# Performance work log

Measured on AMD Instinct MI355X. Metric: run time of the kernel, lower is better.

Reference implementation:

```python
import jax, jax.numpy as jnp
import numpy as np

DIM = 512
HEADS = 8
LF, P = 32, 32
N = LF * P
LOC_DIM = 64  # loc_emd_dim == locf_dim == 64
SCALE = (DIM // HEADS) ** -0.5


def _position_matrix(boxes):
    # boxes: [N,4] x1y1x2y2 -> [N,N,4] relative geometry (relation-network style)
    x1, y1, x2, y2 = jnp.split(boxes, 4, axis=1)  # each [N,1]
    w = x2 - x1 + 1.0
    h = y2 - y1 + 1.0
    cx = 0.5 * (x1 + x2)
    cy = 0.5 * (y1 + y2)
    dx = jnp.log(jnp.maximum(jnp.abs((cx - cx.T) / w), 1e-3))
    dy = jnp.log(jnp.maximum(jnp.abs((cy - cy.T) / h), 1e-3))
    dw = jnp.log(w.T / w)
    dh = jnp.log(h.T / h)
    return jnp.stack([dx, dy, dw, dh], axis=-1)  # [N,N,4]


def _position_embedding(pos_mat, feat_dim=LOC_DIM, wave_length=1000.0):
    # pos_mat: [N,N,4] -> [N,N,feat_dim] sin/cos embedding
    nf = feat_dim // 8
    dim_mat = wave_length ** (jnp.arange(nf, dtype=jnp.float32) * (8.0 / feat_dim))  # [nf]
    div = pos_mat[..., None] * 100.0 / dim_mat  # [N,N,4,nf]
    emb = jnp.concatenate([jnp.sin(div), jnp.cos(div)], axis=-1)  # [N,N,4,2nf]
    return emb.reshape(pos_mat.shape[0], pos_mat.shape[1], feat_dim)


def setup_inputs() -> dict:
    key = jax.random.key(0)
    ks = jax.random.split(key, 8)
    x = jax.random.normal(ks[0], (1, N, DIM), jnp.float32)
    x_reg = jax.random.normal(ks[1], (1, N, DIM), jnp.float32)
    # valid boxes: x1y1x2y2 within a ~1000x600 frame
    cx = jax.random.uniform(ks[2], (LF, P, 1)) * 1000.0
    cy = jax.random.uniform(ks[3], (LF, P, 1)) * 600.0
    w = jax.random.uniform(ks[4], (LF, P, 1)) * 150.0 + 10.0
    h = jax.random.uniform(ks[5], (LF, P, 1)) * 150.0 + 10.0
    locs = jnp.concatenate([cx - w / 2, cy - h / 2, cx + w / 2, cy + h / 2], axis=-1)
    W_qkv = jax.random.normal(ks[6], (3 * DIM, DIM), jnp.float32) * 0.02
    W_loc = jax.random.normal(ks[7], (HEADS, LOC_DIM), jnp.float32) * 0.01  # 1x1 conv weight
    b_loc = jnp.zeros((HEADS,), jnp.float32)
    return {"x": x, "x_reg": x_reg, "locs": locs, "W_qkv": W_qkv, "W_loc": W_loc, "b_loc": b_loc}


def reference(x, x_reg, locs, W_qkv, W_loc, b_loc):
    B, n, C = x.shape
    boxes = locs.reshape(-1, 4)
    # location embedding -> 1x1 conv -> ReLU  (attn_lt: [H,N,N])
    pos_emb = _position_embedding(_position_matrix(boxes), LOC_DIM)  # [N,N,64]
    attn_lt = jax.nn.relu(jnp.einsum('nmf,hf->hnm', pos_emb, W_loc) + b_loc[:, None, None])
    # qkv projection (bias=False)
    qkv = (x @ W_qkv.T).reshape(B, n, 3, HEADS, C // HEADS)
    qkv = jnp.transpose(qkv, (2, 0, 3, 1, 4))  # [3,B,H,N,hd]
    q, k, v = qkv[0], qkv[1], qkv[2]
    attn = jnp.einsum('bhnd,bhmd->bhnm', q, k) * SCALE
    attn = attn + jnp.log(attn_lt + 1e-6)[None]  # loc_fuse_type == 'add'
    attn = jax.nn.softmax(attn, axis=-1)
    out = jnp.einsum('bhnm,bhmd->bhnd', attn, v)
    return jnp.transpose(out, (0, 2, 1, 3)).reshape(B, n, C)
```

## Files before the change

kernel.cpp:

```cpp
#include <hip/hip_runtime.h>
#include <hip/hip_bf16.h>


namespace {
constexpr int NN   = 1024;
constexpr int CDIM = 512;
constexpr int NH   = 8;
constexpr int HD   = 64;
constexpr int NOUT = 3 * CDIM;
constexpr int PROJ_BLOCKS = (NN / 64) * (NOUT / 64);
constexpr float QSCALE = 0.125f;

constexpr size_t QKBF_OFF_U16 = 0;
constexpr size_t VT_OFF_U16   = (size_t)2 * NH * NN * HD;
constexpr size_t XB_OFF_U16   = VT_OFF_U16 + (size_t)NH * HD * NN;
constexpr size_t WB_OFF_U16   = XB_OFF_U16 + (size_t)NN * CDIM;
constexpr size_t L_OFF_U16    = WB_OFF_U16 + (size_t)NOUT * CDIM;
constexpr size_t END_U16      = L_OFF_U16 + (size_t)NH * NN * NN;
constexpr size_t BF_OFF_F32   = END_U16 / 2;
constexpr size_t WR_OFF_F32   = BF_OFF_F32 + 6 * NN;
constexpr size_t W2_OFF_U16   = 2 * (WR_OFF_F32 + 528);
}

typedef __attribute__((ext_vector_type(8))) short short8v;
typedef __attribute__((ext_vector_type(4))) float f32x4;

__device__ __forceinline__ unsigned short f2bf(float f) {
  union { float f; unsigned int u; } v; v.f = f;
  unsigned int u = v.u;
  u += 0x7fffu + ((u >> 16) & 1u);
  return (unsigned short)(u >> 16);
}
__device__ __forceinline__ float b2f(unsigned short u) {
  union { unsigned int u; float f; } v; v.u = ((unsigned int)u) << 16; return v.f;
}

__global__ __launch_bounds__(256) void k_cvt(const float* __restrict__ x,
                                             const float* __restrict__ wq,
                                             const float* __restrict__ locs,
                                             const float* __restrict__ wloc,
                                             const float* __restrict__ bloc,
                                             unsigned short* __restrict__ xb,
                                             unsigned short* __restrict__ wb,
                                             float* __restrict__ bf,
                                             float* __restrict__ wr,
                                             unsigned short* __restrict__ w2) {
  constexpr int XTOT = NN * CDIM;
  constexpr int CVT_BLOCKS = 1280;
  int b = blockIdx.x;
  int tid = threadIdx.x;
  if (b < CVT_BLOCKS) {
    int idx = (b * 256 + tid) * 4;
    if (idx < XTOT) {
      float4 v = *reinterpret_cast<const float4*>(x + idx);
      ushort4 o;
      o.x = f2bf(v.x); o.y = f2bf(v.y); o.z = f2bf(v.z); o.w = f2bf(v.w);
      *reinterpret_cast<ushort4*>(xb + idx) = o;
    } else {
      int j = idx - XTOT;
      float4 v = *reinterpret_cast<const float4*>(wq + j);
      ushort4 o;
      o.x = f2bf(v.x); o.y = f2bf(v.y); o.z = f2bf(v.z); o.w = f2bf(v.w);
      *reinterpret_cast<ushort4*>(wb + j) = o;
    }
  } else {
    for (int i = tid; i < NN; i += 256) {
      float4 b4 = reinterpret_cast<const float4*>(locs)[i];
      float x1 = b4.x, y1 = b4.y, x2 = b4.z, y2 = b4.w;
      float w = x2 - x1 + 1.0f;
      float h = y2 - y1 + 1.0f;
      bf[0 * NN + i] = 0.5f * (x1 + x2);
      bf[1 * NN + i] = 0.5f * (y1 + y2);
      bf[2 * NN + i] = w;
      bf[3 * NN + i] = h;
      bf[4 * NN + i] = logf(w);
      bf[5 * NN + i] = logf(h);
    }
    if (tid < 8) wr[512 + tid] = bloc[tid];
    for (int i = tid; i < 16 * 64; i += 256) {
      int hh = i >> 6, f = i & 63;
      int sc = f & 1, tj = f >> 1, j = tj & 3, t = tj >> 2;
      float v = (hh < 8) ? wloc[hh * 64 + j * 16 + sc * 8 + t] : 0.0f;
      w2[i] = f2bf(v);
    }
  }
}

__global__ __launch_bounds__(256) void k_mid(const unsigned short* __restrict__ xb,
                                             const unsigned short* __restrict__ wb,
                                             unsigned short* __restrict__ qk_bf,
                                             unsigned short* __restrict__ vt,
                                             const float* __restrict__ bf,
                                             const float* __restrict__ wr,
                                             const unsigned short* __restrict__ w2,
                                             unsigned short* __restrict__ L) {
  __shared__ unsigned short A_lds[64][72];
  __shared__ unsigned short B_lds[64][72];
  int blk = blockIdx.x;
  int tid = threadIdx.x;

  if (blk >= PROJ_BLOCKS) {
    int blk2 = blk - PROJ_BLOCKS;
    int n = blk2 >> 2;
    int m0 = (blk2 & 3) * 256;
    int w = tid >> 6, l = tid & 63, g = l >> 4, c = l & 15;

    const float* cx = bf;
    const float* cy = bf + NN;
    const float* lw = bf + 4 * NN;
    const float* lh = bf + 5 * NN;

    float cxn = cx[n], cyn = cy[n];
    float rwn = 1.0f / bf[2 * NN + n];
    float rhn = 1.0f / bf[3 * NN + n];
    float lwn = lw[n], lhn = lh[n];

    float ang0 = 100.0f * exp2f(-1.2457230355894468f * (float)g);
    float ang1 = ang0 * 0.031622776601683794f;

    short8v aw_lo = *reinterpret_cast<const short8v*>(w2 + c * 64 + 8 * g);
    short8v aw_hi = *reinterpret_cast<const short8v*>(w2 + c * 64 + 32 + 8 * g);
    float br_[4];
#pragma unroll
    for (int r = 0; r < 4; ++r) br_[r] = wr[512 + ((4 * g + r) & 7)];

#pragma unroll
    for (int it = 0; it < 4; ++it) {
      int m = m0 + w * 64 + it * 16 + c;
      float dx = __logf(fmaxf(fabsf((cxn - cx[m]) * rwn), 1e-3f));
      float dy = __logf(fmaxf(fabsf((cyn - cy[m]) * rhn), 1e-3f));
      float dwv = lw[m] - lwn;
      float dhv = lh[m] - lhn;
      float pos[4] = {dx, dy, dwv, dhv};

      union BU { unsigned int u[4]; short8v v; } b0, b1;
#pragma unroll
      for (int j = 0; j < 4; ++j) {
        float s0v, c0v, s1v, c1v;
        __sincosf(pos[j] * ang0, &s0v, &c0v);
        __sincosf(pos[j] * ang1, &s1v, &c1v);
        union { __hip_bfloat162 h; unsigned int u; } cv0, cv1;
        cv0.h = __float22bfloat162_rn(make_float2(s0v, c0v));
        cv1.h = __float22bfloat162_rn(make_float2(s1v, c1v));
        b0.u[j] = cv0.u;
        b1.u[j] = cv1.u;
      }

      f32x4 z = {0.f, 0.f, 0.f, 0.f};
      f32x4 acc4 = __builtin_amdgcn_mfma_f32_16x16x32_bf16(aw_lo, b0.v, z, 0, 0, 0);
      acc4 = __builtin_amdgcn_mfma_f32_16x16x32_bf16(aw_hi, b1.v, acc4, 0, 0, 0);

      if (g < 2) {
#pragma unroll
        for (int r = 0; r < 4; ++r) {
          float v = fmaxf(acc4[r] + br_[r], 0.0f) + 1e-6f;
          L[((size_t)(4 * g + r) * NN + n) * NN + m] = f2bf(v);
        }
      }
    }
  } else {
    int t = blk;
    int n0 = (t & 15) * 64, i0 = (t >> 4) * 64;
    int w = tid >> 6, l = tid & 63, g = l >> 4, c = l & 15;
    int sr = tid >> 2;
    int sc = (tid & 3) * 16;

    f32x4 acc[4];
#pragma unroll
    for (int ct = 0; ct < 4; ++ct) acc[ct] = (f32x4){0.f, 0.f, 0.f, 0.f};

    for (int kt = 0; kt < CDIM; kt += 64) {
      const unsigned short* asrc = xb + (size_t)(n0 + sr) * CDIM + kt + sc;
      const unsigned short* bsrc = wb + (size_t)(i0 + sr) * CDIM + kt + sc;
      *reinterpret_cast<short8v*>(&A_lds[sr][sc])     = *reinterpret_cast<const short8v*>(asrc);
      *reinterpret_cast<short8v*>(&A_lds[sr][sc + 8]) = *reinterpret_cast<const short8v*>(asrc + 8);
      *reinterpret_cast<short8v*>(&B_lds[sr][sc])     = *reinterpret_cast<const short8v*>(bsrc);
      *reinterpret_cast<short8v*>(&B_lds[sr][sc + 8]) = *reinterpret_cast<const short8v*>(bsrc + 8);
      __syncthreads();
#pragma unroll
      for (int kks = 0; kks < 2; ++kks) {
        short8v a = *reinterpret_cast<const short8v*>(&A_lds[16 * w + c][kks * 32 + 8 * g]);
#pragma unroll
        for (int ct = 0; ct < 4; ++ct) {
          short8v b = *reinterpret_cast<const short8v*>(&B_lds[16 * ct + c][kks * 32 + 8 * g]);
          acc[ct] = __builtin_amdgcn_mfma_f32_16x16x32_bf16(a, b, acc[ct], 0, 0, 0);
        }
      }
      __syncthreads();
    }

    int s = i0 >> 9;
    int hh = (i0 >> 6) & 7;
    if (s < 2) {
      float scale = (s == 0) ? QSCALE : 1.0f;
      unsigned short* dst = qk_bf + ((size_t)(s * NH + hh) * NN) * HD;
#pragma unroll
      for (int ct = 0; ct < 4; ++ct)
#pragma unroll
        for (int r = 0; r < 4; ++r) {
          int n = n0 + 16 * w + 4 * g + r;
          dst[(size_t)n * HD + 16 * ct + c] = f2bf(acc[ct][r] * scale);
        }
    } else {
#pragma unroll
      for (int ct = 0; ct < 4; ++ct)
#pragma unroll
        for (int r = 0; r < 4; ++r) {
          A_lds[16 * w + 4 * g + r][16 * ct + c] = f2bf(acc[ct][r]);
        }
      __syncthreads();
      int d = tid >> 2;
      int nn0 = (tid & 3) * 16;
      unsigned short o[16];
#pragma unroll
      for (int nn = 0; nn < 16; ++nn) o[nn] = A_lds[nn0 + nn][d];
      unsigned short* dst = vt + ((size_t)hh * HD + d) * NN + n0 + nn0;
      *reinterpret_cast<short8v*>(dst)     = *reinterpret_cast<short8v*>(&o[0]);
      *reinterpret_cast<short8v*>(dst + 8) = *reinterpret_cast<short8v*>(&o[8]);
    }
  }
}

__global__ __launch_bounds__(512) void k_mha(const unsigned short* __restrict__ qk,
                                             const unsigned short* __restrict__ vt,
                                             const unsigned short* __restrict__ L,
                                             float* __restrict__ out) {
  __shared__ short8v smem16[3200];
  auto V = reinterpret_cast<unsigned short(*)[64][40]>(smem16);
  auto P = reinterpret_cast<unsigned short(*)[640]>(
      reinterpret_cast<char*>(smem16) + 40960);
  auto accs = reinterpret_cast<float(*)[16][68]>(smem16);
  auto mls = reinterpret_cast<float(*)[2][16]>(reinterpret_cast<char*>(smem16) + 34816);
  auto scw2 = reinterpret_cast<float(*)[16]>(reinterpret_cast<char*>(smem16) + 35840);
  auto rlf = reinterpret_cast<float*>(reinterpret_cast<char*>(smem16) + 36352);

  int tid = threadIdx.x;
  int w = tid >> 6;
  int l = tid & 63;
  int g = l >> 4;
  int c = l & 15;
  int h = blockIdx.y;
  int n0 = blockIdx.x * 16;

  const unsigned short* qb = qk + ((size_t)(0 * NH + h) * NN + n0) * HD;
  const unsigned short* kb = qk + ((size_t)(1 * NH + h) * NN) * HD;
  const unsigned short* vb = vt + (size_t)h * HD * NN;
  const unsigned short* Lb = L + ((size_t)h * NN + n0 + 4 * g) * NN;

  short8v a_lo = *reinterpret_cast<const short8v*>(qb + (size_t)c * HD + 8 * g);
  short8v a_hi = *reinterpret_cast<const short8v*>(qb + (size_t)c * HD + 32 + 8 * g);

  f32x4 acc[4];
#pragma unroll
  for (int ct = 0; ct < 4; ++ct) acc[ct] = (f32x4){0.f, 0.f, 0.f, 0.f};
  float m_run[4] = {-3.0e38f, -3.0e38f, -3.0e38f, -3.0e38f};
  float l_run[4] = {0.f, 0.f, 0.f, 0.f};

#pragma unroll
  for (int it = 0; it < 4; ++it) {
    int mt = w * 128 + it * 32;

#pragma unroll
    for (int p = 0; p < 4; ++p) {
      int d = p * 16 + (l >> 2);
      int key16 = (l & 3) * 8;
      *reinterpret_cast<short8v*>(&V[w][d][key16]) =
          *reinterpret_cast<const short8v*>(vb + (size_t)d * NN + mt + key16);
    }

    float t0[4], t1[4];
#pragma unroll
    for (int r = 0; r < 4; ++r) {
      t0[r] = b2f(Lb[(size_t)r * NN + mt + c]);
      t1[r] = b2f(Lb[(size_t)r * NN + mt + 16 + c]);
    }

    const unsigned short* k0p = kb + (size_t)(mt + c) * HD + 8 * g;
    const unsigned short* k1p = kb + (size_t)(mt + 16 + c) * HD + 8 * g;
    short8v b0_lo = *reinterpret_cast<const short8v*>(k0p);
    short8v b0_hi = *reinterpret_cast<const short8v*>(k0p + 32);
    short8v b1_lo = *reinterpret_cast<const short8v*>(k1p);
    short8v b1_hi = *reinterpret_cast<const short8v*>(k1p + 32);

    __builtin_amdgcn_s_setprio(1);
    f32x4 z = {0.f, 0.f, 0.f, 0.f};
    f32x4 s0 = __builtin_amdgcn_mfma_f32_16x16x32_bf16(a_lo, b0_lo, z, 0, 0, 0);
    s0 = __builtin_amdgcn_mfma_f32_16x16x32_bf16(a_hi, b0_hi, s0, 0, 0, 0);
    f32x4 s1 = __builtin_amdgcn_mfma_f32_16x16x32_bf16(a_lo, b1_lo, z, 0, 0, 0);
    s1 = __builtin_amdgcn_mfma_f32_16x16x32_bf16(a_hi, b1_hi, s1, 0, 0, 0);
    __builtin_amdgcn_s_setprio(0);

    float sc[4], p0[4], p1[4];
#pragma unroll
    for (int r = 0; r < 4; ++r) {
      float mx = fmaxf(s0[r], s1[r]);
      mx = fmaxf(mx, __shfl_xor(mx, 1));
      mx = fmaxf(mx, __shfl_xor(mx, 2));
      mx = fmaxf(mx, __shfl_xor(mx, 4));
      mx = fmaxf(mx, __shfl_xor(mx, 8));
      float m_new = fmaxf(m_run[r], mx);
      sc[r] = __expf(m_run[r] - m_new);
      p0[r] = t0[r] * __expf(s0[r] - m_new);
      p1[r] = t1[r] * __expf(s1[r] - m_new);
      l_run[r] = l_run[r] * sc[r] + (p0[r] + p1[r]);
      m_run[r] = m_new;
    }
#pragma unroll
    for (int ct = 0; ct < 4; ++ct)
#pragma unroll
      for (int r = 0; r < 4; ++r) acc[ct][r] *= sc[r];

#pragma unroll
    for (int r = 0; r < 4; ++r) {
      P[w][(4 * g + r) * 40 + c] = f2bf(p0[r]);
      P[w][(4 * g + r) * 40 + 16 + c] = f2bf(p1[r]);
    }
    __builtin_amdgcn_wave_barrier();

    short8v pa = *reinterpret_cast<const short8v*>(&P[w][c * 40 + 8 * g]);
    __builtin_amdgcn_s_setprio(1);
#pragma unroll
    for (int ct = 0; ct < 4; ++ct) {
      short8v vbf = *reinterpret_cast<const short8v*>(&V[w][ct * 16 + c][8 * g]);
      acc[ct] = __builtin_amdgcn_mfma_f32_16x16x32_bf16(pa, vbf, acc[ct], 0, 0, 0);
    }
    __builtin_amdgcn_s_setprio(0);
    __builtin_amdgcn_wave_barrier();
  }

#pragma unroll
  for (int r = 0; r < 4; ++r) {
    float ls = l_run[r];
    ls += __shfl_xor(ls, 1);
    ls += __shfl_xor(ls, 2);
    ls += __shfl_xor(ls, 4);
    ls += __shfl_xor(ls, 8);
    l_run[r] = ls;
  }

  __syncthreads();

  if (c == 0) {
#pragma unroll
    for (int r = 0; r < 4; ++r) {
      mls[w][0][4 * g + r] = m_run[r];
      mls[w][1][4 * g + r] = l_run[r];
    }
  }
#pragma unroll
  for (int ct = 0; ct < 4; ++ct)
#pragma unroll
    for (int r = 0; r < 4; ++r) accs[w][4 * g + r][ct * 16 + c] = acc[ct][r];
  __syncthreads();

  if (tid < 16) {
    int row = tid;
    float mfin = mls[0][0][row];
#pragma unroll
    for (int w2i = 1; w2i < 8; ++w2i) mfin = fmaxf(mfin, mls[w2i][0][row]);
    float lfin = 0.f;
#pragma unroll
    for (int w2i = 0; w2i < 8; ++w2i) {
      float scv = __expf(mls[w2i][0][row] - mfin);
      scw2[w2i][row] = scv;
      lfin += mls[w2i][1][row] * scv;
    }
    rlf[row] = 1.0f / lfin;
  }
  __syncthreads();

#pragma unroll
  for (int o = tid; o < 16 * 64; o += 512) {
    int row = o >> 6, col = o & 63;
    float val = 0.f;
#pragma unroll
    for (int w2i = 0; w2i < 8; ++w2i) {
      val += scw2[w2i][row] * accs[w2i][row][col];
    }
    out[(size_t)(n0 + row) * CDIM + h * HD + col] = val * rlf[row];
  }
}

extern "C" void kernel_launch(void* const* d_in, const int* in_sizes, int n_in,
                              void* d_out, int out_size, void* d_ws, size_t ws_size,
                              hipStream_t stream) {
  const float* x    = (const float*)d_in[0];
  const float* locs = (const float*)d_in[2];
  const float* wqkv = (const float*)d_in[3];
  const float* wloc = (const float*)d_in[4];
  const float* bloc = (const float*)d_in[5];
  float* out = (float*)d_out;
  float* ws = (float*)d_ws;
  unsigned short* ws_u16 = (unsigned short*)d_ws;

  unsigned short* qk_bf = ws_u16 + QKBF_OFF_U16;
  unsigned short* vt_bf = ws_u16 + VT_OFF_U16;
  unsigned short* xb    = ws_u16 + XB_OFF_U16;
  unsigned short* wb    = ws_u16 + WB_OFF_U16;
  unsigned short* L     = ws_u16 + L_OFF_U16;
  unsigned short* w2    = ws_u16 + W2_OFF_U16;
  float* bf = ws + BF_OFF_F32;
  float* wr = ws + WR_OFF_F32;

  k_cvt<<<dim3(1281), dim3(256), 0, stream>>>(x, wqkv, locs, wloc, bloc, xb, wb, bf, wr, w2);
  k_mid<<<dim3(PROJ_BLOCKS + 4096), dim3(256), 0, stream>>>(
      xb, wb, qk_bf, vt_bf, bf, wr, w2, L);
  k_mha<<<dim3(NN / 16, NH), dim3(512), 0, stream>>>(qk_bf, vt_bf, L, out);
}
```

Baseline: 50.36 us.

## Merge conversion and mid kernels into one launch with atomic flag dependency

Fuses the fp32-to-bf16 conversion kernel and the projection/location-embedding kernel into a single launch. Projection blocks spin on a global atomic counter until all conversion blocks finish, while location-embedding blocks run independently. Those blocks now compute box geometry and the conv weight layout inline from the raw inputs instead of from a precomputed buffer. The aim is to remove a launch boundary and let the location work overlap the conversion. In exchange it adds a memset, a spin-wait that depends on block scheduling order (the converters have lower block indices), and redundant per-block recomputation of logs and weights.

```diff
diff --git a/kernel.cpp b/kernel.cpp
--- a/kernel.cpp
+++ b/kernel.cpp
@@ -8,6 +8,8 @@
 constexpr int NH   = 8;
 constexpr int HD   = 64;
 constexpr int NOUT = 3 * CDIM;
+constexpr int CVT_BLOCKS  = 1280;
+constexpr int LOC_BLOCKS  = 4096;
 constexpr int PROJ_BLOCKS = (NN / 64) * (NOUT / 64);
 constexpr float QSCALE = 0.125f;
 
@@ -17,9 +19,7 @@
 constexpr size_t WB_OFF_U16   = XB_OFF_U16 + (size_t)NN * CDIM;
 constexpr size_t L_OFF_U16    = WB_OFF_U16 + (size_t)NOUT * CDIM;
 constexpr size_t END_U16      = L_OFF_U16 + (size_t)NH * NN * NN;
-constexpr size_t BF_OFF_F32   = END_U16 / 2;
-constexpr size_t WR_OFF_F32   = BF_OFF_F32 + 6 * NN;
-constexpr size_t W2_OFF_U16   = 2 * (WR_OFF_F32 + 528);
+constexpr size_t FLAG_OFF_B   = END_U16 * 2;
 }
 
 typedef __attribute__((ext_vector_type(8))) short short8v;
@@ -35,22 +35,25 @@
   union { unsigned int u; float f; } v; v.u = ((unsigned int)u) << 16; return v.f;
 }
 
-__global__ __launch_bounds__(256) void k_cvt(const float* __restrict__ x,
-                                             const float* __restrict__ wq,
-                                             const float* __restrict__ locs,
-                                             const float* __restrict__ wloc,
-                                             const float* __restrict__ bloc,
-                                             unsigned short* __restrict__ xb,
-                                             unsigned short* __restrict__ wb,
-                                             float* __restrict__ bf,
-                                             float* __restrict__ wr,
-                                             unsigned short* __restrict__ w2) {
-  constexpr int XTOT = NN * CDIM;
-  constexpr int CVT_BLOCKS = 1280;
-  int b = blockIdx.x;
+__global__ __launch_bounds__(256) void k_union(const float* __restrict__ x,
+                                               const float* __restrict__ wq,
+                                               const float* __restrict__ locs,
+                                               const float* __restrict__ wloc,
+                                               const float* __restrict__ bloc,
+                                               unsigned short* __restrict__ xb,
+                                               unsigned short* __restrict__ wb,
+                                               unsigned short* __restrict__ qk_bf,
+                                               unsigned short* __restrict__ vt,
+                                               unsigned short* __restrict__ L,
+                                               unsigned int* __restrict__ flag) {
+  __shared__ unsigned short A_lds[64][72];
+  __shared__ unsigned short B_lds[64][72];
+  int blk = blockIdx.x;
   int tid = threadIdx.x;
-  if (b < CVT_BLOCKS) {
-    int idx = (b * 256 + tid) * 4;
+
+  if (blk < CVT_BLOCKS) {
+    constexpr int XTOT = NN * CDIM;
+    int idx = (blk * 256 + tid) * 4;
     if (idx < XTOT) {
       float4 v = *reinterpret_cast<const float4*>(x + idx);
       ushort4 o;
@@ -63,74 +66,56 @@
       o.x = f2bf(v.x); o.y = f2bf(v.y); o.z = f2bf(v.z); o.w = f2bf(v.w);
       *reinterpret_cast<ushort4*>(wb + j) = o;
     }
-  } else {
-    for (int i = tid; i < NN; i += 256) {
-      float4 b4 = reinterpret_cast<const float4*>(locs)[i];
-      float x1 = b4.x, y1 = b4.y, x2 = b4.z, y2 = b4.w;
-      float w = x2 - x1 + 1.0f;
-      float h = y2 - y1 + 1.0f;
-      bf[0 * NN + i] = 0.5f * (x1 + x2);
-      bf[1 * NN + i] = 0.5f * (y1 + y2);
-      bf[2 * NN + i] = w;
-      bf[3 * NN + i] = h;
-      bf[4 * NN + i] = logf(w);
-      bf[5 * NN + i] = logf(h);
-    }
-    if (tid < 8) wr[512 + tid] = bloc[tid];
-    for (int i = tid; i < 16 * 64; i += 256) {
-      int hh = i >> 6, f = i & 63;
-      int sc = f & 1, tj = f >> 1, j = tj & 3, t = tj >> 2;
-      float v = (hh < 8) ? wloc[hh * 64 + j * 16 + sc * 8 + t] : 0.0f;
-      w2[i] = f2bf(v);
-    }
-  }
-}
-
-__global__ __launch_bounds__(256) void k_mid(const unsigned short* __restrict__ xb,
-                                             const unsigned short* __restrict__ wb,
-                                             unsigned short* __restrict__ qk_bf,
-                                             unsigned short* __restrict__ vt,
-                                             const float* __restrict__ bf,
-                                             const float* __restrict__ wr,
-                                             const unsigned short* __restrict__ w2,
-                                             unsigned short* __restrict__ L) {
-  __shared__ unsigned short A_lds[64][72];
-  __shared__ unsigned short B_lds[64][72];
-  int blk = blockIdx.x;
-  int tid = threadIdx.x;
-
-  if (blk >= PROJ_BLOCKS) {
-    int blk2 = blk - PROJ_BLOCKS;
+    __threadfence();
+    __syncthreads();
+    if (tid == 0) {
+      __hip_atomic_fetch_add(flag, 1u, __ATOMIC_RELEASE, __HIP_MEMORY_SCOPE_AGENT);
+    }
+  } else if (blk < CVT_BLOCKS + LOC_BLOCKS) {
+    int blk2 = blk - CVT_BLOCKS;
     int n = blk2 >> 2;
     int m0 = (blk2 & 3) * 256;
     int w = tid >> 6, l = tid & 63, g = l >> 4, c = l & 15;
 
-    const float* cx = bf;
-    const float* cy = bf + NN;
-    const float* lw = bf + 4 * NN;
-    const float* lh = bf + 5 * NN;
-
-    float cxn = cx[n], cyn = cy[n];
-    float rwn = 1.0f / bf[2 * NN + n];
-    float rhn = 1.0f / bf[3 * NN + n];
-    float lwn = lw[n], lhn = lh[n];
+    float4 bn = reinterpret_cast<const float4*>(locs)[n];
+    float wn = bn.z - bn.x + 1.0f;
+    float hn = bn.w - bn.y + 1.0f;
+    float cxn = 0.5f * (bn.x + bn.z);
+    float cyn = 0.5f * (bn.y + bn.w);
+    float rwn = 1.0f / wn;
+    float rhn = 1.0f / hn;
+    float lwn = __logf(wn);
+    float lhn = __logf(hn);
 
     float ang0 = 100.0f * exp2f(-1.2457230355894468f * (float)g);
     float ang1 = ang0 * 0.031622776601683794f;
 
-    short8v aw_lo = *reinterpret_cast<const short8v*>(w2 + c * 64 + 8 * g);
-    short8v aw_hi = *reinterpret_cast<const short8v*>(w2 + c * 64 + 32 + 8 * g);
+    union AU { unsigned short us[8]; short8v v; } alo, ahi;
+#pragma unroll
+    for (int e = 0; e < 8; ++e) {
+      int f0 = 8 * g + e;
+      int f1 = 32 + 8 * g + e;
+      int sc0 = f0 & 1, j0 = (f0 >> 1) & 3, tt0 = f0 >> 3;
+      int sc1 = f1 & 1, j1 = (f1 >> 1) & 3, tt1 = f1 >> 3;
+      alo.us[e] = (c < 8) ? f2bf(wloc[c * 64 + j0 * 16 + sc0 * 8 + tt0]) : (unsigned short)0;
+      ahi.us[e] = (c < 8) ? f2bf(wloc[c * 64 + j1 * 16 + sc1 * 8 + tt1]) : (unsigned short)0;
+    }
     float br_[4];
 #pragma unroll
-    for (int r = 0; r < 4; ++r) br_[r] = wr[512 + ((4 * g + r) & 7)];
+    for (int r = 0; r < 4; ++r) br_[r] = bloc[(4 * g + r) & 7];
 
 #pragma unroll
     for (int it = 0; it < 4; ++it) {
       int m = m0 + w * 64 + it * 16 + c;
-      float dx = __logf(fmaxf(fabsf((cxn - cx[m]) * rwn), 1e-3f));
-      float dy = __logf(fmaxf(fabsf((cyn - cy[m]) * rhn), 1e-3f));
-      float dwv = lw[m] - lwn;
-      float dhv = lh[m] - lhn;
+      float4 bm = reinterpret_cast<const float4*>(locs)[m];
+      float wm = bm.z - bm.x + 1.0f;
+      float hm = bm.w - bm.y + 1.0f;
+      float cxm = 0.5f * (bm.x + bm.z);
+      float cym = 0.5f * (bm.y + bm.w);
+      float dx = __logf(fmaxf(fabsf((cxn - cxm) * rwn), 1e-3f));
+      float dy = __logf(fmaxf(fabsf((cyn - cym) * rhn), 1e-3f));
+      float dwv = __logf(wm) - lwn;
+      float dhv = __logf(hm) - lhn;
       float pos[4] = {dx, dy, dwv, dhv};
 
       union BU { unsigned int u[4]; short8v v; } b0, b1;
@@ -147,8 +132,8 @@
       }
 
       f32x4 z = {0.f, 0.f, 0.f, 0.f};
-      f32x4 acc4 = __builtin_amdgcn_mfma_f32_16x16x32_bf16(aw_lo, b0.v, z, 0, 0, 0);
-      acc4 = __builtin_amdgcn_mfma_f32_16x16x32_bf16(aw_hi, b1.v, acc4, 0, 0, 0);
+      f32x4 acc4 = __builtin_amdgcn_mfma_f32_16x16x32_bf16(alo.v, b0.v, z, 0, 0, 0);
+      acc4 = __builtin_amdgcn_mfma_f32_16x16x32_bf16(ahi.v, b1.v, acc4, 0, 0, 0);
 
       if (g < 2) {
 #pragma unroll
@@ -159,7 +144,12 @@
       }
     }
   } else {
-    int t = blk;
+    while (__hip_atomic_load(flag, __ATOMIC_ACQUIRE, __HIP_MEMORY_SCOPE_AGENT)
+           < (unsigned int)CVT_BLOCKS) {
+      __builtin_amdgcn_s_sleep(8);
+    }
+
+    int t = blk - (CVT_BLOCKS + LOC_BLOCKS);
     int n0 = (t & 15) * 64, i0 = (t >> 4) * 64;
     int w = tid >> 6, l = tid & 63, g = l >> 4, c = l & 15;
     int sr = tid >> 2;
@@ -390,7 +380,6 @@
   const float* wloc = (const float*)d_in[4];
   const float* bloc = (const float*)d_in[5];
   float* out = (float*)d_out;
-  float* ws = (float*)d_ws;
   unsigned short* ws_u16 = (unsigned short*)d_ws;
 
   unsigned short* qk_bf = ws_u16 + QKBF_OFF_U16;
@@ -398,12 +387,10 @@
   unsigned short* xb    = ws_u16 + XB_OFF_U16;
   unsigned short* wb    = ws_u16 + WB_OFF_U16;
   unsigned short* L     = ws_u16 + L_OFF_U16;
-  unsigned short* w2    = ws_u16 + W2_OFF_U16;
-  float* bf = ws + BF_OFF_F32;
-  float* wr = ws + WR_OFF_F32;
-
-  k_cvt<<<dim3(1281), dim3(256), 0, stream>>>(x, wqkv, locs, wloc, bloc, xb, wb, bf, wr, w2);
-  k_mid<<<dim3(PROJ_BLOCKS + 4096), dim3(256), 0, stream>>>(
-      xb, wb, qk_bf, vt_bf, bf, wr, w2, L);
+  unsigned int* flag    = (unsigned int*)((char*)d_ws + FLAG_OFF_B);
+
+  hipMemsetAsync(flag, 0, sizeof(unsigned int), stream);
+  k_union<<<dim3(CVT_BLOCKS + LOC_BLOCKS + PROJ_BLOCKS), dim3(256), 0, stream>>>(
+      x, wqkv, locs, wloc, bloc, xb, wb, qk_bf, vt_bf, L, flag);
   k_mha<<<dim3(NN / 16, NH), dim3(512), 0, stream>>>(qk_bf, vt_bf, L, out);
 }
```

Result: slower. 184.6 us (+266.5%).
